# Performance work log

Measured on AMD Instinct MI355X. Metric: run time of the kernel, lower is better.

## Reference

```python
import jax, jax.numpy as jnp
import numpy as np

CELL_SIDE = 0.5
N_GRID = 6          # grid side -> 36 occupancy bins
HIDDEN = 128
N_AGENTS = 8192


def setup_inputs() -> dict:
    key = jax.random.key(0)
    k1, k2 = jax.random.split(key, 2)
    # agent (x, y) positions spread over a few meters
    obs = jax.random.normal(k1, (N_AGENTS, 2), dtype=jnp.float32) * 2.0
    W = jax.random.normal(k2, (N_GRID * N_GRID, HIDDEN), dtype=jnp.float32) * 0.1
    b = jnp.zeros((HIDDEN,), dtype=jnp.float32)
    return {"obs": obs, "W": W, "b": b}


def occupancies(obs):
    """Vectorized all-agents occupancy grids. obs: [N, 2] -> [N, g*g]."""
    n_agents = obs.shape[0]
    g = N_GRID
    # relative cell coordinates of every other agent w.r.t. each agent: [N, N, 2]
    rel = (obs[None, :, :] - obs[:, None, :]) / CELL_SIDE + g / 2
    in_range = jnp.all((rel >= 0) & (rel < g), axis=-1)              # [N, N]
    self_ok = ~jnp.isnan(obs[:, 0])                                   # agent with NaN -> zero row
    other_ok = ~jnp.isnan(obs[:, 0])                                  # NaN others filtered out
    not_self = ~jnp.eye(n_agents, dtype=bool)                         # one_cold: exclude self
    valid = in_range & not_self & self_ok[:, None] & other_ok[None, :]
    # .long() in torch truncates; values are >= 0 after the range filter so floor == trunc
    oij = jnp.floor(rel).astype(jnp.int32)                            # [N, N, 2]
    idx = oij[..., 0] * g + oij[..., 1]                               # [N, N]
    idx = jnp.where(valid, idx, g * g)                                # dump invalid into slot g*g
    rows = jnp.arange(n_agents)[:, None]
    occ = jnp.zeros((n_agents, g * g + 1), dtype=obs.dtype)
    occ = occ.at[rows, idx].set(1.0)                                  # occ[oi] = 1 (duplicates fine)
    return occ[:, : g * g]


def reference(obs, W, b):
    occ = occupancies(obs)          # [N, 36]
    return occ @ W + b              # [N, 128]
```

## Files before the change

### kernel.cpp

```cpp
#include <hip/hip_runtime.h>

#define NAG    8192
#define CHUNK  256
#define NCHUNK (NAG / CHUNK)
#define GG     36
#define HID    128

__global__ __launch_bounds__(256) void occ_pair_masks(
    const float* __restrict__ obs, unsigned long long* __restrict__ partials) {
  const int t     = threadIdx.x;
  const int agent = blockIdx.x * 256 + t;
  const int jbase = blockIdx.y * CHUNK;

  __shared__ float2 pj[CHUNK];

  const float2* obs2 = (const float2*)obs;
  float2 p = obs2[jbase + t];
  pj[t] = make_float2(p.x * 2.0f, p.y * 2.0f);

  const float2 myp = obs2[agent];
  const float bx = 3.0f - myp.x * 2.0f;
  const float by = 3.0f - myp.y * 2.0f;

  __syncthreads();

  unsigned long long mask = 0ull;
  #pragma unroll 8
  for (int jj = 0; jj < CHUNK; ++jj) {
    const float rx = pj[jj].x + bx;
    const float ry = pj[jj].y + by;
    const int ix = (int)rx;
    const int iy = (int)ry;
    const bool valid = (rx >= 0.0f) & (ry >= 0.0f) &
                       ((unsigned)ix < 6u) & ((unsigned)iy < 6u) &
                       ((jbase + jj) != agent);
    const int bitpos = valid ? (ix * 6 + iy) : 63;
    mask |= (1ull << bitpos);
  }
  partials[blockIdx.y * NAG + agent] = mask & ((1ull << GG) - 1ull);
}

__global__ __launch_bounds__(256) void occ_matmul(
    const unsigned long long* __restrict__ partials,
    const float* __restrict__ W, const float* __restrict__ b,
    float* __restrict__ out) {
  const int t     = threadIdx.x;
  const int lane  = t & 31;
  const int agent = blockIdx.x * 8 + (t >> 5);

  unsigned long long m = partials[lane * NAG + agent];
  #pragma unroll
  for (int s = 16; s; s >>= 1) m |= __shfl_xor(m, s, 32);

  const unsigned mlo = (unsigned)m;
  const unsigned mhi = (unsigned)(m >> 32);

  const float4* W4 = (const float4*)W;
  float4 acc = ((const float4*)b)[lane];

  #pragma unroll
  for (int c = 0; c < GG; ++c) {
    const unsigned bit = (c < 32) ? ((mlo >> c) & 1u) : ((mhi >> (c - 32)) & 1u);
    const float sel = (float)bit;
    const float4 w = W4[c * 32 + lane];
    acc.x = fmaf(sel, w.x, acc.x);
    acc.y = fmaf(sel, w.y, acc.y);
    acc.z = fmaf(sel, w.z, acc.z);
    acc.w = fmaf(sel, w.w, acc.w);
  }
  ((float4*)out)[agent * 32 + lane] = acc;
}

extern "C" void kernel_launch(void* const* d_in, const int* in_sizes, int n_in,
                              void* d_out, int out_size, void* d_ws, size_t ws_size,
                              hipStream_t stream) {
  const float* obs = (const float*)d_in[0];
  const float* W   = (const float*)d_in[1];
  const float* b   = (const float*)d_in[2];
  float* out = (float*)d_out;
  unsigned long long* partials = (unsigned long long*)d_ws;

  occ_pair_masks<<<dim3(NAG / 256, NCHUNK), 256, 0, stream>>>(obs, partials);
  occ_matmul<<<dim3(NAG / 8), 256, 0, stream>>>(partials, W, b, out);
}
```

Measured before the change: 91.93 us.

## Register-block four agents per thread and drop self-check off diagonal tiles

Each thread now handles four agents against a 128-wide j chunk, so every shared-memory load of a neighbour position is reused across four pair tests. The self-exclusion compare runs only in diagonal tiles, and the bin index moves to a shift/or 8x8 layout instead of a multiply-add. The matmul kernel now ORs 64 partial masks (two per lane) and remaps bits to the 6x6 order. This doubles the partials written and read, and raises register pressure per thread.

```diff
diff --git a/kernel.cpp b/kernel.cpp
--- a/kernel.cpp
+++ b/kernel.cpp
@@ -1,43 +1,85 @@
 #include <hip/hip_runtime.h>
 
-#define NAG    8192
-#define CHUNK  256
-#define NCHUNK (NAG / CHUNK)
-#define GG     36
-#define HID    128
+#define NAG  8192
+#define JCH  128
+#define NCH  (NAG / JCH)
+#define IBLK 1024
+#define GG   36
+#define HID  128
+
+#define PAIR(QX, QY, BX, BY, M)                                          \
+  {                                                                      \
+    const float rx = (QX) + (BX);                                        \
+    const float ry = (QY) + (BY);                                        \
+    const int ix = (int)rx;             \
+    const int iy = (int)ry;                                              \
+    const bool v = (rx >= 0.0f) & (ry >= 0.0f) &                         \
+                   ((unsigned)ix < 6u) & ((unsigned)iy < 6u);            \
+    const int bp = v ? (((ix & 7) << 3) | (iy & 7)) : 63;                \
+    (M) |= (1ull << bp);                                                 \
+  }
+
+#define PAIR_NS(QX, QY, BX, BY, M, J, I)                                 \
+  {                                                                      \
+    const float rx = (QX) + (BX);                                        \
+    const float ry = (QY) + (BY);                                        \
+    const int ix = (int)rx;                                              \
+    const int iy = (int)ry;                                              \
+    const bool v = (rx >= 0.0f) & (ry >= 0.0f) &                         \
+                   ((unsigned)ix < 6u) & ((unsigned)iy < 6u) &           \
+                   ((J) != (I));                                         \
+    const int bp = v ? (((ix & 7) << 3) | (iy & 7)) : 63;                \
+    (M) |= (1ull << bp);                                                 \
+  }
 
 __global__ __launch_bounds__(256) void occ_pair_masks(
     const float* __restrict__ obs, unsigned long long* __restrict__ partials) {
-  const int t     = threadIdx.x;
-  const int agent = blockIdx.x * 256 + t;
-  const int jbase = blockIdx.y * CHUNK;
+  const int t  = threadIdx.x;
+  const int bx = blockIdx.x, by = blockIdx.y;
+  const int i0 = bx * IBLK + t * 4;
+  const int jbase = by * JCH;
 
-  __shared__ float2 pj[CHUNK];
+  __shared__ float2 pj[JCH];
+  if (t < JCH) {
+    const float2 q = ((const float2*)obs)[jbase + t];
+    pj[t] = make_float2(q.x * 2.0f, q.y * 2.0f);
+  }
 
-  const float2* obs2 = (const float2*)obs;
-  float2 p = obs2[jbase + t];
-  pj[t] = make_float2(p.x * 2.0f, p.y * 2.0f);
-
-  const float2 myp = obs2[agent];
-  const float bx = 3.0f - myp.x * 2.0f;
-  const float by = 3.0f - myp.y * 2.0f;
+  const float4* obs4 = (const float4*)obs;
+  const float4 A = obs4[i0 / 2];
+  const float4 B = obs4[i0 / 2 + 1];
+  const float bx0 = 3.0f - A.x * 2.0f, by0 = 3.0f - A.y * 2.0f;
+  const float bx1 = 3.0f - A.z * 2.0f, by1 = 3.0f - A.w * 2.0f;
+  const float bx2 = 3.0f - B.x * 2.0f, by2 = 3.0f - B.y * 2.0f;
+  const float bx3 = 3.0f - B.z * 2.0f, by3 = 3.0f - B.w * 2.0f;
 
   __syncthreads();
 
-  unsigned long long mask = 0ull;
-  #pragma unroll 8
-  for (int jj = 0; jj < CHUNK; ++jj) {
-    const float rx = pj[jj].x + bx;
-    const float ry = pj[jj].y + by;
-    const int ix = (int)rx;
-    const int iy = (int)ry;
-    const bool valid = (rx >= 0.0f) & (ry >= 0.0f) &
-                       ((unsigned)ix < 6u) & ((unsigned)iy < 6u) &
-                       ((jbase + jj) != agent);
-    const int bitpos = valid ? (ix * 6 + iy) : 63;
-    mask |= (1ull << bitpos);
+  unsigned long long m0 = 0, m1 = 0, m2 = 0, m3 = 0;
+
+  if ((by >> 3) != bx) {
+    #pragma unroll 4
+    for (int jj = 0; jj < JCH; ++jj) {
+      const float qx = pj[jj].x, qy = pj[jj].y;
+      PAIR(qx, qy, bx0, by0, m0)
+      PAIR(qx, qy, bx1, by1, m1)
+      PAIR(qx, qy, bx2, by2, m2)
+      PAIR(qx, qy, bx3, by3, m3)
+    }
+  } else {
+    #pragma unroll 4
+    for (int jj = 0; jj < JCH; ++jj) {
+      const float qx = pj[jj].x, qy = pj[jj].y;
+      const int j = jbase + jj;
+      PAIR_NS(qx, qy, bx0, by0, m0, j, i0 + 0)
+      PAIR_NS(qx, qy, bx1, by1, m1, j, i0 + 1)
+      PAIR_NS(qx, qy, bx2, by2, m2, j, i0 + 2)
+      PAIR_NS(qx, qy, bx3, by3, m3, j, i0 + 3)
+    }
   }
-  partials[blockIdx.y * NAG + agent] = mask & ((1ull << GG) - 1ull);
+
+  unsigned long long* p = partials + (size_t)by * NAG + i0;
+  p[0] = m0; p[1] = m1; p[2] = m2; p[3] = m3;
 }
 
 __global__ __launch_bounds__(256) void occ_matmul(
@@ -48,7 +90,8 @@
   const int lane  = t & 31;
   const int agent = blockIdx.x * 8 + (t >> 5);
 
-  unsigned long long m = partials[lane * NAG + agent];
+  unsigned long long m = partials[(size_t)lane * NAG + agent] |
+                         partials[(size_t)(lane + 32) * NAG + agent];
   #pragma unroll
   for (int s = 16; s; s >>= 1) m |= __shfl_xor(m, s, 32);
 
@@ -60,13 +103,15 @@
 
   #pragma unroll
   for (int c = 0; c < GG; ++c) {
-    const unsigned bit = (c < 32) ? ((mlo >> c) & 1u) : ((mhi >> (c - 32)) & 1u);
-    const float sel = (float)bit;
+    const int bit = (c / 6) * 8 + (c % 6);
+    const unsigned sel =
+        (bit < 32) ? ((mlo >> bit) & 1u) : ((mhi >> (bit - 32)) & 1u);
+    const float s = (float)sel;
     const float4 w = W4[c * 32 + lane];
-    acc.x = fmaf(sel, w.x, acc.x);
-    acc.y = fmaf(sel, w.y, acc.y);
-    acc.z = fmaf(sel, w.z, acc.z);
-    acc.w = fmaf(sel, w.w, acc.w);
+    acc.x = fmaf(s, w.x, acc.x);
+    acc.y = fmaf(s, w.y, acc.y);
+    acc.z = fmaf(s, w.z, acc.z);
+    acc.w = fmaf(s, w.w, acc.w);
   }
   ((float4*)out)[agent * 32 + lane] = acc;
 }
@@ -80,6 +125,6 @@
   float* out = (float*)d_out;
   unsigned long long* partials = (unsigned long long*)d_ws;
 
-  occ_pair_masks<<<dim3(NAG / 256, NCHUNK), 256, 0, stream>>>(obs, partials);
+  occ_pair_masks<<<dim3(NAG / IBLK, NCH), 256, 0, stream>>>(obs, partials);
   occ_matmul<<<dim3(NAG / 8), 256, 0, stream>>>(partials, W, b, out);
 }
```

New measurement: 96.33 us. 4.8% more time.
